# Kernel tuning notes

Hardware: AMD Instinct MI355X
Metric: run time of the kernel (lower is better)

The kernel has to match this reference:

```python
import jax, jax.numpy as jnp
import numpy as np

B, T, N, F_IN, F_OUT, K = 4, 32, 1024, 128, 128, 4


def setup_inputs() -> dict:
    key = jax.random.key(0)
    k1, k2, k3 = jax.random.split(key, 3)
    X = jax.random.normal(k1, (B, T, N, F_IN), dtype=jnp.float32)
    # graph-shift operator; 1/sqrt(N) scaling keeps S^k products numerically tame
    S = jax.random.normal(k2, (N, N), dtype=jnp.float32) / np.float32(np.sqrt(N))
    W = jax.random.normal(k3, (F_OUT, F_IN, K), dtype=jnp.float32) * 0.1
    b = jnp.zeros((F_OUT,), dtype=jnp.float32)
    return {"X": X, "S": S, "W": W, "b": b}


def reference(X, S, W, b):
    # Y[:, t] = sum_{k=0}^{K-1, t-k>=0} S^k @ X[:, t-k] @ W[:, :, k]^T + b
    # (static graph: the per-(t,k) shift-chain product in the original collapses to S^k)
    Bsz, Tlen, Nn, Fin = X.shape
    Kord = W.shape[-1]
    Y = jnp.zeros((Bsz, Tlen, Nn, W.shape[0]), X.dtype)
    Z = X  # Z = S^k @ X, starting at k=0 (identity)
    for k in range(Kord):
        # causal time-shift by k: output at t uses Z at t-k (zeros for t-k<0)
        Zs = Z if k == 0 else jnp.pad(Z, ((0, 0), (k, 0), (0, 0), (0, 0)))[:, :Tlen]
        Y = Y + jnp.einsum('btnf,of->btno', Zs, W[:, :, k])
        if k < Kord - 1:
            Z = jnp.einsum('nm,btmf->btnf', S, Z)  # advance shift power
    return Y + b
```

## Files before the change

kernel.cpp:

```cpp
#include <hip/hip_runtime.h>
#include <stdint.h>

#define BT 128
#define NN 1024
#define FF 128

typedef __attribute__((ext_vector_type(8))) short short8;
typedef __attribute__((ext_vector_type(4))) float float4v;
typedef __attribute__((ext_vector_type(4))) unsigned short ushort4v;

__device__ __forceinline__ unsigned short f2bf(float f) {
  uint32_t u = __builtin_bit_cast(uint32_t, f);
  u += 0x7FFFu + ((u >> 16) & 1u);
  return (unsigned short)(u >> 16);
}

__device__ __forceinline__ void gload16(const void* g, void* l) {
  __builtin_amdgcn_global_load_lds(
      (const __attribute__((address_space(1))) uint32_t*)(g),
      (__attribute__((address_space(3))) uint32_t*)(l),
      16, 0, 0);
}

__global__ __launch_bounds__(256) void k_cvt_sw(const float* __restrict__ S,
                                                unsigned short* __restrict__ Sbf,
                                                const float* __restrict__ W,
                                                unsigned short* __restrict__ Wk2,
                                                unsigned short* __restrict__ zbuf) {
  int tid = threadIdx.x;
  int b = blockIdx.x;
  if (b < 64) {
#pragma unroll
    for (int i = 0; i < 16; ++i) {
      int g4 = b * 4096 + i * 256 + tid;
      float4v v = reinterpret_cast<const float4v*>(S)[g4];
      ushort4v h;
      h[0] = f2bf(v[0]); h[1] = f2bf(v[1]); h[2] = f2bf(v[2]); h[3] = f2bf(v[3]);
      reinterpret_cast<ushort4v*>(Sbf)[g4] = h;
    }
  } else if (b < 320) {
    int gid = (b - 64) * 256 + tid;
    int k = gid >> 14, o = (gid >> 7) & 127, f = gid & 127;
    Wk2[gid] = f2bf(W[(o * 128 + f) * 4 + k]);
  } else {
    ushort4v z = (ushort4v){0, 0, 0, 0};
#pragma unroll
    for (int i = 0; i < 16; ++i)
      reinterpret_cast<ushort4v*>(zbuf)[(b - 320) * 4096 + i * 256 + tid] = z;
  }
}

__global__ __launch_bounds__(256) void k_cvt_x(const float* __restrict__ X,
                                               unsigned short* __restrict__ Xbf) {
  int base = blockIdx.x * 1024 + threadIdx.x;
#pragma unroll
  for (int i = 0; i < 4; ++i) {
    int g4 = base + i * 256;
    float4v v = reinterpret_cast<const float4v*>(X)[g4];
    ushort4v h;
    h[0] = f2bf(v[0]); h[1] = f2bf(v[1]); h[2] = f2bf(v[2]); h[3] = f2bf(v[3]);
    reinterpret_cast<ushort4v*>(Xbf)[g4] = h;
  }
}

__global__ __launch_bounds__(256) void k_proj(const unsigned short* __restrict__ Wk2,
                                              const unsigned short* __restrict__ Xbf,
                                              unsigned short* __restrict__ U3) {
  __shared__ unsigned short lA[128 * 64];
  __shared__ unsigned short lB[128 * 64];
  int bt = blockIdx.x >> 3;
  int n0 = (blockIdx.x & 7) << 7;
  int tid = threadIdx.x;
  int wave = tid >> 6, lane = tid & 63;
  int wr = wave >> 1, wc = wave & 1;
  int lr = lane & 15, g = lane >> 4;

  const unsigned short* gA = Wk2 + 3 * (FF * FF);
  const unsigned short* gB = Xbf + (size_t)bt * (NN * FF) + (size_t)n0 * FF;

  float4v acc[4][4];
#pragma unroll
  for (int a = 0; a < 4; ++a)
#pragma unroll
    for (int b = 0; b < 4; ++b) acc[a][b] = (float4v){0.f, 0.f, 0.f, 0.f};

  for (int kt = 0; kt < 2; ++kt) {
    int m0 = kt * 64;
#pragma unroll
    for (int i = 0; i < 4; ++i) {
      int id = i * 256 + tid;
      int row = id >> 3;
      int mc = (id & 7) << 3;
      int slot = (i * 256 + (tid & 192)) * 8;
      gload16(gA + (size_t)row * 128 + m0 + mc, &lA[slot]);
      gload16(gB + (size_t)row * 128 + m0 + mc, &lB[slot]);
    }
    __syncthreads();
#pragma unroll
    for (int kk = 0; kk < 2; ++kk) {
      short8 aF[4], bF[4];
#pragma unroll
      for (int mi = 0; mi < 4; ++mi)
        aF[mi] = *reinterpret_cast<const short8*>(
            &lA[(wr * 64 + mi * 16 + lr) * 64 + kk * 32 + g * 8]);
#pragma unroll
      for (int ni = 0; ni < 4; ++ni)
        bF[ni] = *reinterpret_cast<const short8*>(
            &lB[(wc * 64 + ni * 16 + lr) * 64 + kk * 32 + g * 8]);
#pragma unroll
      for (int mi = 0; mi < 4; ++mi)
#pragma unroll
        for (int ni = 0; ni < 4; ++ni)
          acc[mi][ni] = __builtin_amdgcn_mfma_f32_16x16x32_bf16(
              aF[mi], bF[ni], acc[mi][ni], 0, 0, 0);
    }
    __syncthreads();
  }

  unsigned short* Uo = U3 + (size_t)bt * (NN * FF);
#pragma unroll
  for (int mi = 0; mi < 4; ++mi) {
#pragma unroll
    for (int ni = 0; ni < 4; ++ni) {
      int o = wr * 64 + mi * 16 + g * 4;
      int n = n0 + wc * 64 + ni * 16 + lr;
#pragma unroll
      for (int j = 0; j < 4; ++j)
        Uo[(size_t)(o + j) * NN + n] = f2bf(acc[mi][ni][j]);
    }
  }
}

template <bool FINAL>
__global__ __launch_bounds__(512, 2) void k_chain(
    const unsigned short* __restrict__ Uin,
    const unsigned short* __restrict__ Sbf,
    const unsigned short* __restrict__ Wg,
    const unsigned short* __restrict__ Xbf,
    const unsigned short* __restrict__ zbuf,
    unsigned short* __restrict__ Hout,
    float* __restrict__ Yout,
    const float* __restrict__ bias) {
  extern __shared__ unsigned char lds[];

  int bid = blockIdx.x;
  int logical = (bid & 7) * 32 + (bid >> 3);
  int cblk = logical >> 2;
  int nblk = logical & 3;

  int tid = threadIdx.x;
  int wave = tid >> 6, lane = tid & 63;
  int wave_m = wave >> 2, wave_n = wave & 3;
  int lr = lane & 15, g = lane >> 4;

  const int bt0 = cblk * 2;
  const bool t0z = ((bt0 & 31) == 0);
  const unsigned short* A0 = t0z ? zbuf : (Uin + (size_t)(bt0 - 1) * (NN * FF));
  const unsigned short* A1 = Uin + (size_t)bt0 * (NN * FF);

  const unsigned short* pS[4][2];
  unsigned dstO[4][2];
#pragma unroll
  for (int j = 0; j < 2; ++j) {
    int sr0 = wave * 16 + j * 8;
    int rbA = (sr0 & 63) + ((sr0 >> 6) << 7);
    int rbB = (sr0 & 31) + ((sr0 >> 5) << 6);
    int seg = lane & 7;
    int rA0 = rbA + (lane >> 3), rA1 = rA0 + 64;
    int rB0 = rbB + (lane >> 3), rB1 = rB0 + 32;
    pS[0][j] = (rA0 < 128 ? A0 + (size_t)rA0 * NN : A1 + (size_t)(rA0 - 128) * NN)
               + ((seg ^ (rA0 & 7)) << 3);
    pS[3][j] = (rA1 < 128 ? A0 + (size_t)rA1 * NN : A1 + (size_t)(rA1 - 128) * NN)
               + ((seg ^ (rA1 & 7)) << 3);
    pS[1][j] = Sbf + (size_t)(nblk * 256 + rB0) * NN + ((seg ^ (rB0 & 7)) << 3);
    pS[2][j] = Sbf + (size_t)(nblk * 256 + rB1) * NN + ((seg ^ (rB1 & 7)) << 3);
    dstO[0][j] = (unsigned)rbA * 128u;
    dstO[3][j] = (unsigned)(rbA + 64) * 128u;
    dstO[1][j] = 32768u + (unsigned)rbB * 128u;
    dstO[2][j] = 32768u + (unsigned)(rbB + 32) * 128u;
  }

  const unsigned xm = (unsigned)((lr & 7) << 4);
  const unsigned xo0 = ((unsigned)(g * 16)) ^ xm;
  const unsigned xo1 = ((unsigned)(64 + g * 16)) ^ xm;
  const unsigned aRB = (unsigned)((wave_m * 128 + lr) * 128);
  const unsigned bRB = 32768u + (unsigned)((wave_n * 64 + lr) * 128);

#define RD(OFF) (*reinterpret_cast<const short8*>(lds + (OFF)))

  float4v acc[8][4];
#pragma unroll
  for (int a = 0; a < 8; ++a)
#pragma unroll
    for (int b = 0; b < 4; ++b) acc[a][b] = (float4v){0.f, 0.f, 0.f, 0.f};

  short8 aX[4], aY[4], nB0[4], nB1[4];

#pragma unroll
  for (int s = 0; s < 4; ++s)
#pragma unroll
    for (int j = 0; j < 2; ++j) gload16(pS[s][j], lds + dstO[s][j]);
  asm volatile("s_waitcnt vmcnt(0)" ::: "memory");
  __builtin_amdgcn_s_barrier();

  for (int kt = 0; kt < 16; ++kt) {
    const unsigned bo = (unsigned)(kt & 1) << 16;
    const unsigned nbo = bo ^ 65536u;
    const unsigned ko = (unsigned)(kt + 1) * 64u;
    const bool st = (kt < 15);

#pragma unroll
    for (int mf = 0; mf < 4; ++mf) aX[mf] = RD(bo + aRB + (unsigned)mf * 2048u + xo0);
#pragma unroll
    for (int nf = 0; nf < 4; ++nf) nB0[nf] = RD(bo + bRB + (unsigned)nf * 2048u + xo0);
    if (st) {
      gload16(pS[0][0] + ko, lds + nbo + dstO[0][0]);
      gload16(pS[0][1] + ko, lds + nbo + dstO[0][1]);
      asm volatile("s_waitcnt vmcnt(4)" ::: "memory");
    }
    __builtin_amdgcn_s_barrier();
    asm volatile("s_waitcnt lgkmcnt(0)" ::: "memory");
    __builtin_amdgcn_sched_barrier(0);
    __builtin_amdgcn_s_setprio(1);
#pragma unroll
    for (int mf = 0; mf < 4; ++mf)
#pragma unroll
      for (int nf = 0; nf < 4; ++nf)
        acc[mf][nf] = __builtin_amdgcn_mfma_f32_16x16x32_bf16(aX[mf], nB0[nf], acc[mf][nf], 0, 0, 0);
    __builtin_amdgcn_s_setprio(0);
    __builtin_amdgcn_sched_barrier(0);
    __builtin_amdgcn_s_barrier();
    __builtin_amdgcn_sched_barrier(0);

#pragma unroll
    for (int mf = 0; mf < 4; ++mf) aY[mf] = RD(bo + aRB + (unsigned)mf * 2048u + xo1);
#pragma unroll
    for (int nf = 0; nf < 4; ++nf) nB1[nf] = RD(bo + bRB + (unsigned)nf * 2048u + xo1);
    if (st) {
      gload16(pS[1][0] + ko, lds + nbo + dstO[1][0]);
      gload16(pS[1][1] + ko, lds + nbo + dstO[1][1]);
      asm volatile("s_waitcnt vmcnt(4)" ::: "memory");
    } else {
      asm volatile("s_waitcnt vmcnt(0)" ::: "memory");
    }
    __builtin_amdgcn_s_barrier();
    asm volatile("s_waitcnt lgkmcnt(0)" ::: "memory");
    __builtin_amdgcn_sched_barrier(0);
    __builtin_amdgcn_s_setprio(1);
#pragma unroll
    for (int mf = 0; mf < 4; ++mf)
#pragma unroll
      for (int nf = 0; nf < 4; ++nf)
        acc[mf][nf] = __builtin_amdgcn_mfma_f32_16x16x32_bf16(aY[mf], nB1[nf], acc[mf][nf], 0, 0, 0);
    __builtin_amdgcn_s_setprio(0);
    __builtin_amdgcn_sched_barrier(0);
    __builtin_amdgcn_s_barrier();
    __builtin_amdgcn_sched_barrier(0);

#pragma unroll
    for (int mf = 0; mf < 4; ++mf) aX[mf] = RD(bo + aRB + 8192u + (unsigned)mf * 2048u + xo0);
    if (st) {
      gload16(pS[2][0] + ko, lds + nbo + dstO[2][0]);
      gload16(pS[2][1] + ko, lds + nbo + dstO[2][1]);
    }
    __builtin_amdgcn_s_barrier();
    asm volatile("s_waitcnt lgkmcnt(0)" ::: "memory");
    __builtin_amdgcn_sched_barrier(0);
    __builtin_amdgcn_s_setprio(1);
#pragma unroll
    for (int mf = 0; mf < 4; ++mf)
#pragma unroll
      for (int nf = 0; nf < 4; ++nf)
        acc[4 + mf][nf] = __builtin_amdgcn_mfma_f32_16x16x32_bf16(aX[mf], nB0[nf], acc[4 + mf][nf], 0, 0, 0);
    __builtin_amdgcn_s_setprio(0);
    __builtin_amdgcn_sched_barrier(0);
    __builtin_amdgcn_s_barrier();
    __builtin_amdgcn_sched_barrier(0);

#pragma unroll
    for (int mf = 0; mf < 4; ++mf) aY[mf] = RD(bo + aRB + 8192u + (unsigned)mf * 2048u + xo1);
    if (st) {
      gload16(pS[3][0] + ko, lds + nbo + dstO[3][0]);
      gload16(pS[3][1] + ko, lds + nbo + dstO[3][1]);
      asm volatile("s_waitcnt vmcnt(2)" ::: "memory");
    }
    __builtin_amdgcn_s_barrier();
    asm volatile("s_waitcnt lgkmcnt(0)" ::: "memory");
    __builtin_amdgcn_sched_barrier(0);
    __builtin_amdgcn_s_setprio(1);
#pragma unroll
    for (int mf = 0; mf < 4; ++mf)
#pragma unroll
      for (int nf = 0; nf < 4; ++nf)
        acc[4 + mf][nf] = __builtin_amdgcn_mfma_f32_16x16x32_bf16(aY[mf], nB1[nf], acc[4 + mf][nf], 0, 0, 0);
    __builtin_amdgcn_s_setprio(0);
    __builtin_amdgcn_sched_barrier(0);
    __builtin_amdgcn_s_barrier();
    __builtin_amdgcn_sched_barrier(0);
  }
#undef RD

  int bt = bt0 + wave_m;
  const unsigned short* Xb = Xbf + (size_t)bt * (NN * FF);
  const int nbase = nblk * 256 + wave_n * 64;
#pragma unroll 1
  for (int kk = 0; kk < 4; ++kk) {
    int fc = kk * 32 + g * 8;
    short8 aW[8], bW[4];
#pragma unroll
    for (int mf = 0; mf < 8; ++mf)
      aW[mf] = *reinterpret_cast<const short8*>(Wg + (size_t)(mf * 16 + lr) * FF + fc);
#pragma unroll
    for (int nf = 0; nf < 4; ++nf)
      bW[nf] = *reinterpret_cast<const short8*>(Xb + (size_t)(nbase + nf * 16 + lr) * FF + fc);
#pragma unroll
    for (int mf = 0; mf < 8; ++mf)
#pragma unroll
      for (int nf = 0; nf < 4; ++nf)
        acc[mf][nf] = __builtin_amdgcn_mfma_f32_16x16x32_bf16(aW[mf], bW[nf], acc[mf][nf], 0, 0, 0);
  }

  if constexpr (FINAL) {
    float* Yp = Yout + (size_t)bt * (NN * FF);
#pragma unroll
    for (int i = 0; i < 8; ++i) {
      int o0 = i * 16 + g * 4;
      float4v bv = *reinterpret_cast<const float4v*>(bias + o0);
#pragma unroll
      for (int j2 = 0; j2 < 4; ++j2) {
        int n = nbase + j2 * 16 + lr;
        float4v r = acc[i][j2] + bv;
        *reinterpret_cast<float4v*>(Yp + (size_t)n * FF + o0) = r;
      }
    }
  } else {
    unsigned short* Hp = Hout + (size_t)bt * (NN * FF);
#pragma unroll
    for (int i = 0; i < 8; ++i) {
      int o0 = i * 16 + g * 4;
#pragma unroll
      for (int j2 = 0; j2 < 4; ++j2) {
        int n = nbase + j2 * 16 + lr;
#pragma unroll
        for (int j = 0; j < 4; ++j)
          Hp[(size_t)(o0 + j) * NN + n] = f2bf(acc[i][j2][j]);
      }
    }
  }
}


extern "C" void kernel_launch(void* const* d_in, const int* in_sizes, int n_in,
                              void* d_out, int out_size, void* d_ws, size_t ws_size,
                              hipStream_t stream) {
  const float* X = (const float*)d_in[0];
  const float* S = (const float*)d_in[1];
  const float* W = (const float*)d_in[2];
  const float* bvec = (const float*)d_in[3];
  float* Y = (float*)d_out;

  char* ws = (char*)d_ws;
  const size_t ZB = (size_t)BT * NN * FF * sizeof(unsigned short);
  unsigned short* Xbf = (unsigned short*)(ws + 0 * ZB);
  unsigned short* U3  = (unsigned short*)(ws + 1 * ZB);
  unsigned short* H2  = (unsigned short*)(ws + 2 * ZB);
  unsigned short* H1  = (unsigned short*)(ws + 3 * ZB);
  unsigned short* Sbf = (unsigned short*)(ws + 4 * ZB);
  unsigned short* Wk2 = (unsigned short*)(ws + 4 * ZB + (size_t)2097152);
  unsigned short* zbf = (unsigned short*)(ws + 4 * ZB + (size_t)2097152 + 131072);

  k_cvt_sw<<<dim3(328), dim3(256), 0, stream>>>(S, Sbf, W, Wk2, zbf);
  k_cvt_x<<<dim3(4096), dim3(256), 0, stream>>>(X, Xbf);
  k_proj<<<dim3(1024), dim3(256), 0, stream>>>(Wk2, Xbf, U3);

  hipError_t e0 = hipFuncSetAttribute((const void*)k_chain<false>,
                      hipFuncAttributeMaxDynamicSharedMemorySize, 131072);
  hipError_t e1 = hipFuncSetAttribute((const void*)k_chain<true>,
                      hipFuncAttributeMaxDynamicSharedMemorySize, 131072);
  (void)e0; (void)e1;

  k_chain<false><<<dim3(256), dim3(512), 131072, stream>>>(
      U3, Sbf, Wk2 + 2 * (FF * FF), Xbf, zbf, H2, nullptr, nullptr);
  k_chain<false><<<dim3(256), dim3(512), 131072, stream>>>(
      H2, Sbf, Wk2 + 1 * (FF * FF), Xbf, zbf, H1, nullptr, nullptr);
  k_chain<true><<<dim3(256), dim3(512), 131072, stream>>>(
      H1, Sbf, Wk2, Xbf, zbf, nullptr, Y, bvec);
}
```

Before: 179.6 us.

## Split k_chain work across 16 waves with smaller per-wave accumulator tiles

Raises the k_chain block from 512 to 1024 threads and halves each wave's M-tile from 128 to 64 rows, so every wave holds 16 accumulator fragments instead of 32. The global-to-LDS staging addressing and the four-phase pipeline are reworked so each wave issues one load per phase. This aims to lower register pressure and add more waves to hide latency. In exchange it adds barrier overhead across 16 waves and gives each wave less MFMA work per LDS read.

```diff
diff --git a/kernel.cpp b/kernel.cpp
--- a/kernel.cpp
+++ b/kernel.cpp
@@ -132,7 +132,7 @@
 }
 
 template <bool FINAL>
-__global__ __launch_bounds__(512, 2) void k_chain(
+__global__ __launch_bounds__(1024, 4) void k_chain(
     const unsigned short* __restrict__ Uin,
     const unsigned short* __restrict__ Sbf,
     const unsigned short* __restrict__ Wg,
@@ -158,48 +158,39 @@
   const unsigned short* A0 = t0z ? zbuf : (Uin + (size_t)(bt0 - 1) * (NN * FF));
   const unsigned short* A1 = Uin + (size_t)bt0 * (NN * FF);
 
-  const unsigned short* pS[4][2];
-  unsigned dstO[4][2];
-#pragma unroll
-  for (int j = 0; j < 2; ++j) {
-    int sr0 = wave * 16 + j * 8;
-    int rbA = (sr0 & 63) + ((sr0 >> 6) << 7);
-    int rbB = (sr0 & 31) + ((sr0 >> 5) << 6);
-    int seg = lane & 7;
-    int rA0 = rbA + (lane >> 3), rA1 = rA0 + 64;
-    int rB0 = rbB + (lane >> 3), rB1 = rB0 + 32;
-    pS[0][j] = (rA0 < 128 ? A0 + (size_t)rA0 * NN : A1 + (size_t)(rA0 - 128) * NN)
-               + ((seg ^ (rA0 & 7)) << 3);
-    pS[3][j] = (rA1 < 128 ? A0 + (size_t)rA1 * NN : A1 + (size_t)(rA1 - 128) * NN)
-               + ((seg ^ (rA1 & 7)) << 3);
-    pS[1][j] = Sbf + (size_t)(nblk * 256 + rB0) * NN + ((seg ^ (rB0 & 7)) << 3);
-    pS[2][j] = Sbf + (size_t)(nblk * 256 + rB1) * NN + ((seg ^ (rB1 & 7)) << 3);
-    dstO[0][j] = (unsigned)rbA * 128u;
-    dstO[3][j] = (unsigned)(rbA + 64) * 128u;
-    dstO[1][j] = 32768u + (unsigned)rbB * 128u;
-    dstO[2][j] = 32768u + (unsigned)(rbB + 32) * 128u;
-  }
+  const int rbe = ((wave * 8) & 31) + ((wave >> 2) << 6);
+  const unsigned laneOff = (unsigned)((lane >> 3) * NN) +
+                           (unsigned)(((lane & 7) ^ ((lane >> 3) & 7)) << 3);
+  const unsigned short* baseAe =
+      (wave < 8) ? (A0 + (size_t)rbe * NN) : (A1 + (size_t)(rbe - 128) * NN);
+  const unsigned short* baseAo = baseAe + 32 * NN;
+  const unsigned short* baseBe = Sbf + (size_t)(nblk * 256 + rbe) * NN;
+  const unsigned short* baseBo = baseBe + 32 * NN;
+  const unsigned dAe = (unsigned)rbe * 128u;
+  const unsigned dAo = dAe + 4096u;
+  const unsigned dBe = 32768u + (unsigned)rbe * 128u;
+  const unsigned dBo = dBe + 4096u;
 
   const unsigned xm = (unsigned)((lr & 7) << 4);
   const unsigned xo0 = ((unsigned)(g * 16)) ^ xm;
   const unsigned xo1 = ((unsigned)(64 + g * 16)) ^ xm;
-  const unsigned aRB = (unsigned)((wave_m * 128 + lr) * 128);
+  const unsigned aRB = (unsigned)((wave_m * 64 + lr) * 128);
   const unsigned bRB = 32768u + (unsigned)((wave_n * 64 + lr) * 128);
 
 #define RD(OFF) (*reinterpret_cast<const short8*>(lds + (OFF)))
 
-  float4v acc[8][4];
-#pragma unroll
-  for (int a = 0; a < 8; ++a)
+  float4v acc[4][4];
+#pragma unroll
+  for (int a = 0; a < 4; ++a)
 #pragma unroll
     for (int b = 0; b < 4; ++b) acc[a][b] = (float4v){0.f, 0.f, 0.f, 0.f};
 
-  short8 aX[4], aY[4], nB0[4], nB1[4];
-
-#pragma unroll
-  for (int s = 0; s < 4; ++s)
-#pragma unroll
-    for (int j = 0; j < 2; ++j) gload16(pS[s][j], lds + dstO[s][j]);
+  short8 aF[2], bF[4];
+
+  gload16(baseBe + laneOff, lds + dBe);
+  gload16(baseBo + laneOff, lds + dBo);
+  gload16(baseAe + laneOff, lds + dAe);
+  gload16(baseAo + laneOff, lds + dAo);
   asm volatile("s_waitcnt vmcnt(0)" ::: "memory");
   __builtin_amdgcn_s_barrier();
 
@@ -209,37 +200,13 @@
     const unsigned ko = (unsigned)(kt + 1) * 64u;
     const bool st = (kt < 15);
 
-#pragma unroll
-    for (int mf = 0; mf < 4; ++mf) aX[mf] = RD(bo + aRB + (unsigned)mf * 2048u + xo0);
-#pragma unroll
-    for (int nf = 0; nf < 4; ++nf) nB0[nf] = RD(bo + bRB + (unsigned)nf * 2048u + xo0);
+    aF[0] = RD(bo + aRB + xo0);
+    aF[1] = RD(bo + aRB + 2048u + xo0);
+#pragma unroll
+    for (int nf = 0; nf < 4; ++nf) bF[nf] = RD(bo + bRB + (unsigned)nf * 2048u + xo0);
     if (st) {
-      gload16(pS[0][0] + ko, lds + nbo + dstO[0][0]);
-      gload16(pS[0][1] + ko, lds + nbo + dstO[0][1]);
-      asm volatile("s_waitcnt vmcnt(4)" ::: "memory");
-    }
-    __builtin_amdgcn_s_barrier();
-    asm volatile("s_waitcnt lgkmcnt(0)" ::: "memory");
-    __builtin_amdgcn_sched_barrier(0);
-    __builtin_amdgcn_s_setprio(1);
-#pragma unroll
-    for (int mf = 0; mf < 4; ++mf)
-#pragma unroll
-      for (int nf = 0; nf < 4; ++nf)
-        acc[mf][nf] = __builtin_amdgcn_mfma_f32_16x16x32_bf16(aX[mf], nB0[nf], acc[mf][nf], 0, 0, 0);
-    __builtin_amdgcn_s_setprio(0);
-    __builtin_amdgcn_sched_barrier(0);
-    __builtin_amdgcn_s_barrier();
-    __builtin_amdgcn_sched_barrier(0);
-
-#pragma unroll
-    for (int mf = 0; mf < 4; ++mf) aY[mf] = RD(bo + aRB + (unsigned)mf * 2048u + xo1);
-#pragma unroll
-    for (int nf = 0; nf < 4; ++nf) nB1[nf] = RD(bo + bRB + (unsigned)nf * 2048u + xo1);
-    if (st) {
-      gload16(pS[1][0] + ko, lds + nbo + dstO[1][0]);
-      gload16(pS[1][1] + ko, lds + nbo + dstO[1][1]);
-      asm volatile("s_waitcnt vmcnt(4)" ::: "memory");
+      gload16(baseBe + laneOff + ko, lds + nbo + dBe);
+      asm volatile("s_waitcnt vmcnt(1)" ::: "memory");
     } else {
       asm volatile("s_waitcnt vmcnt(0)" ::: "memory");
     }
@@ -248,73 +215,89 @@
     __builtin_amdgcn_sched_barrier(0);
     __builtin_amdgcn_s_setprio(1);
 #pragma unroll
-    for (int mf = 0; mf < 4; ++mf)
-#pragma unroll
-      for (int nf = 0; nf < 4; ++nf)
-        acc[mf][nf] = __builtin_amdgcn_mfma_f32_16x16x32_bf16(aY[mf], nB1[nf], acc[mf][nf], 0, 0, 0);
+    for (int nf = 0; nf < 4; ++nf) {
+      acc[0][nf] = __builtin_amdgcn_mfma_f32_16x16x32_bf16(aF[0], bF[nf], acc[0][nf], 0, 0, 0);
+      acc[1][nf] = __builtin_amdgcn_mfma_f32_16x16x32_bf16(aF[1], bF[nf], acc[1][nf], 0, 0, 0);
+    }
     __builtin_amdgcn_s_setprio(0);
     __builtin_amdgcn_sched_barrier(0);
     __builtin_amdgcn_s_barrier();
     __builtin_amdgcn_sched_barrier(0);
 
-#pragma unroll
-    for (int mf = 0; mf < 4; ++mf) aX[mf] = RD(bo + aRB + 8192u + (unsigned)mf * 2048u + xo0);
+    aF[0] = RD(bo + aRB + 4096u + xo0);
+    aF[1] = RD(bo + aRB + 6144u + xo0);
+    if (st) gload16(baseBo + laneOff + ko, lds + nbo + dBo);
+    __builtin_amdgcn_s_barrier();
+    asm volatile("s_waitcnt lgkmcnt(0)" ::: "memory");
+    __builtin_amdgcn_sched_barrier(0);
+    __builtin_amdgcn_s_setprio(1);
+#pragma unroll
+    for (int nf = 0; nf < 4; ++nf) {
+      acc[2][nf] = __builtin_amdgcn_mfma_f32_16x16x32_bf16(aF[0], bF[nf], acc[2][nf], 0, 0, 0);
+      acc[3][nf] = __builtin_amdgcn_mfma_f32_16x16x32_bf16(aF[1], bF[nf], acc[3][nf], 0, 0, 0);
+    }
+    __builtin_amdgcn_s_setprio(0);
+    __builtin_amdgcn_sched_barrier(0);
+    __builtin_amdgcn_s_barrier();
+    __builtin_amdgcn_sched_barrier(0);
+
+    aF[0] = RD(bo + aRB + xo1);
+    aF[1] = RD(bo + aRB + 2048u + xo1);
+#pragma unroll
+    for (int nf = 0; nf < 4; ++nf) bF[nf] = RD(bo + bRB + (unsigned)nf * 2048u + xo1);
+    if (st) gload16(baseAe + laneOff + ko, lds + nbo + dAe);
+    __builtin_amdgcn_s_barrier();
+    asm volatile("s_waitcnt lgkmcnt(0)" ::: "memory");
+    __builtin_amdgcn_sched_barrier(0);
+    __builtin_amdgcn_s_setprio(1);
+#pragma unroll
+    for (int nf = 0; nf < 4; ++nf) {
+      acc[0][nf] = __builtin_amdgcn_mfma_f32_16x16x32_bf16(aF[0], bF[nf], acc[0][nf], 0, 0, 0);
+      acc[1][nf] = __builtin_amdgcn_mfma_f32_16x16x32_bf16(aF[1], bF[nf], acc[1][nf], 0, 0, 0);
+    }
+    __builtin_amdgcn_s_setprio(0);
+    __builtin_amdgcn_sched_barrier(0);
+    __builtin_amdgcn_s_barrier();
+    __builtin_amdgcn_sched_barrier(0);
+
+    aF[0] = RD(bo + aRB + 4096u + xo1);
+    aF[1] = RD(bo + aRB + 6144u + xo1);
     if (st) {
-      gload16(pS[2][0] + ko, lds + nbo + dstO[2][0]);
-      gload16(pS[2][1] + ko, lds + nbo + dstO[2][1]);
+      gload16(baseAo + laneOff + ko, lds + nbo + dAo);
+      asm volatile("s_waitcnt vmcnt(1)" ::: "memory");
     }
     __builtin_amdgcn_s_barrier();
     asm volatile("s_waitcnt lgkmcnt(0)" ::: "memory");
     __builtin_amdgcn_sched_barrier(0);
     __builtin_amdgcn_s_setprio(1);
 #pragma unroll
-    for (int mf = 0; mf < 4; ++mf)
-#pragma unroll
-      for (int nf = 0; nf < 4; ++nf)
-        acc[4 + mf][nf] = __builtin_amdgcn_mfma_f32_16x16x32_bf16(aX[mf], nB0[nf], acc[4 + mf][nf], 0, 0, 0);
+    for (int nf = 0; nf < 4; ++nf) {
+      acc[2][nf] = __builtin_amdgcn_mfma_f32_16x16x32_bf16(aF[0], bF[nf], acc[2][nf], 0, 0, 0);
+      acc[3][nf] = __builtin_amdgcn_mfma_f32_16x16x32_bf16(aF[1], bF[nf], acc[3][nf], 0, 0, 0);
+    }
     __builtin_amdgcn_s_setprio(0);
     __builtin_amdgcn_sched_barrier(0);
     __builtin_amdgcn_s_barrier();
     __builtin_amdgcn_sched_barrier(0);
-
-#pragma unroll
-    for (int mf = 0; mf < 4; ++mf) aY[mf] = RD(bo + aRB + 8192u + (unsigned)mf * 2048u + xo1);
-    if (st) {
-      gload16(pS[3][0] + ko, lds + nbo + dstO[3][0]);
-      gload16(pS[3][1] + ko, lds + nbo + dstO[3][1]);
-      asm volatile("s_waitcnt vmcnt(2)" ::: "memory");
-    }
-    __builtin_amdgcn_s_barrier();
-    asm volatile("s_waitcnt lgkmcnt(0)" ::: "memory");
-    __builtin_amdgcn_sched_barrier(0);
-    __builtin_amdgcn_s_setprio(1);
-#pragma unroll
-    for (int mf = 0; mf < 4; ++mf)
-#pragma unroll
-      for (int nf = 0; nf < 4; ++nf)
-        acc[4 + mf][nf] = __builtin_amdgcn_mfma_f32_16x16x32_bf16(aY[mf], nB1[nf], acc[4 + mf][nf], 0, 0, 0);
-    __builtin_amdgcn_s_setprio(0);
-    __builtin_amdgcn_sched_barrier(0);
-    __builtin_amdgcn_s_barrier();
-    __builtin_amdgcn_sched_barrier(0);
   }
 #undef RD
 
-  int bt = bt0 + wave_m;
+  const int bt = bt0 + (wave_m >> 1);
+  const int oh = (wave_m & 1) * 64;
   const unsigned short* Xb = Xbf + (size_t)bt * (NN * FF);
   const int nbase = nblk * 256 + wave_n * 64;
 #pragma unroll 1
   for (int kk = 0; kk < 4; ++kk) {
     int fc = kk * 32 + g * 8;
-    short8 aW[8], bW[4];
-#pragma unroll
-    for (int mf = 0; mf < 8; ++mf)
-      aW[mf] = *reinterpret_cast<const short8*>(Wg + (size_t)(mf * 16 + lr) * FF + fc);
+    short8 aW[4], bW[4];
+#pragma unroll
+    for (int mf = 0; mf < 4; ++mf)
+      aW[mf] = *reinterpret_cast<const short8*>(Wg + (size_t)(oh + mf * 16 + lr) * FF + fc);
 #pragma unroll
     for (int nf = 0; nf < 4; ++nf)
       bW[nf] = *reinterpret_cast<const short8*>(Xb + (size_t)(nbase + nf * 16 + lr) * FF + fc);
 #pragma unroll
-    for (int mf = 0; mf < 8; ++mf)
+    for (int mf = 0; mf < 4; ++mf)
 #pragma unroll
       for (int nf = 0; nf < 4; ++nf)
         acc[mf][nf] = __builtin_amdgcn_mfma_f32_16x16x32_bf16(aW[mf], bW[nf], acc[mf][nf], 0, 0, 0);
@@ -323,27 +306,27 @@
   if constexpr (FINAL) {
     float* Yp = Yout + (size_t)bt * (NN * FF);
 #pragma unroll
-    for (int i = 0; i < 8; ++i) {
-      int o0 = i * 16 + g * 4;
+    for (int mf = 0; mf < 4; ++mf) {
+      int o0 = oh + mf * 16 + g * 4;
       float4v bv = *reinterpret_cast<const float4v*>(bias + o0);
 #pragma unroll
-      for (int j2 = 0; j2 < 4; ++j2) {
-        int n = nbase + j2 * 16 + lr;
-        float4v r = acc[i][j2] + bv;
+      for (int nf = 0; nf < 4; ++nf) {
+        int n = nbase + nf * 16 + lr;
+        float4v r = acc[mf][nf] + bv;
         *reinterpret_cast<float4v*>(Yp + (size_t)n * FF + o0) = r;
       }
     }
   } else {
     unsigned short* Hp = Hout + (size_t)bt * (NN * FF);
 #pragma unroll
-    for (int i = 0; i < 8; ++i) {
-      int o0 = i * 16 + g * 4;
-#pragma unroll
-      for (int j2 = 0; j2 < 4; ++j2) {
-        int n = nbase + j2 * 16 + lr;
+    for (int mf = 0; mf < 4; ++mf) {
+      int o0 = oh + mf * 16 + g * 4;
+#pragma unroll
+      for (int nf = 0; nf < 4; ++nf) {
+        int n = nbase + nf * 16 + lr;
 #pragma unroll
         for (int j = 0; j < 4; ++j)
-          Hp[(size_t)(o0 + j) * NN + n] = f2bf(acc[i][j2][j]);
+          Hp[(size_t)(o0 + j) * NN + n] = f2bf(acc[mf][nf][j]);
       }
     }
   }
@@ -379,10 +362,10 @@
                       hipFuncAttributeMaxDynamicSharedMemorySize, 131072);
   (void)e0; (void)e1;
 
-  k_chain<false><<<dim3(256), dim3(512), 131072, stream>>>(
+  k_chain<false><<<dim3(256), dim3(1024), 131072, stream>>>(
       U3, Sbf, Wk2 + 2 * (FF * FF), Xbf, zbf, H2, nullptr, nullptr);
-  k_chain<false><<<dim3(256), dim3(512), 131072, stream>>>(
+  k_chain<false><<<dim3(256), dim3(1024), 131072, stream>>>(
       H2, Sbf, Wk2 + 1 * (FF * FF), Xbf, zbf, H1, nullptr, nullptr);
-  k_chain<true><<<dim3(256), dim3(512), 131072, stream>>>(
+  k_chain<true><<<dim3(256), dim3(1024), 131072, stream>>>(
       H1, Sbf, Wk2, Xbf, zbf, nullptr, Y, bvec);
 }
```

Measured after the change: 184.3 us. 1.03x slower.
